# Kernel optimization log

Measured on AMD Instinct MI355X. Metric: run time of the kernel, lower is better.

The kernel has to match this reference:

```python
import jax, jax.numpy as jnp
import numpy as np

CODEBOOK_SIZE = 8192
CODEBOOK_DIM = 16
IN_DIM = 512


def setup_inputs() -> dict:
    key = jax.random.key(0)
    k1, k2, k3 = jax.random.split(key, 3)
    input_values = jax.random.normal(k1, (8, 4096, IN_DIM), dtype=jnp.float32)
    # xavier_uniform for Linear(IN_DIM -> CODEBOOK_DIM), weight shape (out, in) in torch
    limit = float(np.sqrt(6.0 / (IN_DIM + CODEBOOK_DIM)))
    proj_weight = jax.random.uniform(k2, (CODEBOOK_DIM, IN_DIM), dtype=jnp.float32, minval=-limit, maxval=limit)
    code_book = jax.random.normal(k3, (CODEBOOK_SIZE, CODEBOOK_DIM), dtype=jnp.float32)
    return {"input_values": input_values, "proj_weight": proj_weight, "code_book": code_book}


def reference(input_values, proj_weight, code_book):
    # targets: (B, L, d) = input @ W^T  (bias-free random projection)
    targets = jnp.einsum("bld,cd->blc", input_values, proj_weight)  # (B, L, 16)
    # Squared L2 distance via expansion ||t - c||^2 = ||t||^2 - 2 t.c + ||c||^2.
    # argmin is identical to argmin of the norm; avoids the (B,L,K,d) broadcast tensor.
    t_sq = jnp.sum(targets * targets, axis=-1, keepdims=True)        # (B, L, 1)
    c_sq = jnp.sum(code_book * code_book, axis=-1)                   # (K,)
    cross = jnp.einsum("blc,kc->blk", targets, code_book)            # (B, L, K)
    dist_sq = t_sq - 2.0 * cross + c_sq                              # (B, L, K)
    labels = jnp.argmin(dist_sq, axis=-1)                            # (B, L) int
    return labels
```

## Files before the change

### kernel.cpp

```cpp
#include <hip/hip_runtime.h>
#include <stdint.h>

#define IN_DIM 512
#define CB 8192
#define CD 16
#define NROWS 32768
#define DELTAQ 8e-3f
#define FMAXV 3.402823466e38f
#define FBB 4

typedef short bf16x8 __attribute__((ext_vector_type(8)));
typedef float f32x4 __attribute__((ext_vector_type(4)));

__device__ inline unsigned short f2bf(float x) {
    unsigned u = __float_as_uint(x);
    unsigned r = u + 0x7FFFu + ((u >> 16) & 1u);
    return (unsigned short)(r >> 16);
}
__device__ inline float bf2f(unsigned short h) { return __uint_as_float(((unsigned)h) << 16); }
__device__ inline unsigned umin32(unsigned a, unsigned b) { return a < b ? a : b; }
__device__ inline unsigned umax32(unsigned a, unsigned b) { return a > b ? a : b; }
__device__ inline unsigned long long shfl_xor_u64(unsigned long long x, int m) {
    double d = __shfl_xor(__longlong_as_double((long long)x), m, 64);
    return (unsigned long long)__double_as_longlong(d);
}
__device__ inline unsigned med3_u32(unsigned a, unsigned b, unsigned c) {
    unsigned d;
    asm("v_med3_u32 %0, %1, %2, %3" : "=v"(d) : "v"(a), "v"(b), "v"(c));
    return d;
}

__global__ __launch_bounds__(256) void prep_kernel(const float* __restrict__ cb,
                                                   float* __restrict__ csq,
                                                   f32x4* __restrict__ csq4,
                                                   bf16x8* __restrict__ Bp,
                                                   int* __restrict__ counter) {
    int id = blockIdx.x * 256 + threadIdx.x;
    if (id == 0) counter[0] = 0;
    if (id < CB) {
        const float4* p = (const float4*)(cb + (size_t)id * CD);
        float s = 0.f;
#pragma unroll
        for (int j = 0; j < 4; ++j) {
            float4 v = p[j];
            s += v.x * v.x + v.y * v.y + v.z * v.z + v.w * v.w;
        }
        csq[id] = s;
        float so = s + 256.0f;
        f32x4 v4 = {so, so, so, so};
        csq4[id] = v4;
    }
    int slot = id & 63;
    int nt = id >> 6;
    int q = slot >> 4;
    int n = nt * 16 + (slot & 15);
    int d0 = (q & 1) * 8;
    bool lo = (q < 2);
    const float* src = cb + (size_t)n * CD + d0;
    bf16x8 v;
#pragma unroll
    for (int j = 0; j < 8; ++j) {
        float x = src[j];
        unsigned short a = f2bf(x);
        unsigned short b = f2bf(x - bf2f(a));
        v[j] = (short)(lo ? a : b);
    }
    Bp[id] = v;
}

__global__ __launch_bounds__(512, 4) void fused_kernel(
        const float* __restrict__ in, const float* __restrict__ W,
        float* __restrict__ tpout, const f32x4* __restrict__ csq4,
        const bf16x8* __restrict__ Bp, int* __restrict__ out,
        int* __restrict__ queue, int* __restrict__ counter) {
    __shared__ float4 LIN[2048];
    __shared__ float4 WL[16 * 129];
    __shared__ float tbuf[64][17];
    __shared__ unsigned long long m_k[64][8];
    __shared__ unsigned m_s2[64][8];

    int tid = threadIdx.x;
    int lane = tid & 63;
    int wv = __builtin_amdgcn_readfirstlane(tid >> 6);
    int rowbase = blockIdx.x * 64;
    const float4* inp4 = (const float4*)in;
    const float4* W4 = (const float4*)W;

#pragma unroll
    for (int u = 0; u < 4; ++u) {
        int f = tid + u * 512;
        int d = f >> 7, k = f & 127;
        WL[d * 129 + k] = W4[(size_t)d * 128 + k];
    }

    float fold0 = 0.f, fold1 = 0.f;
    for (int c = 0; c < 4; ++c) {
        __syncthreads();
#pragma unroll
        for (int u = 0; u < 4; ++u) {
            int f = tid + u * 512;
            int o = f & 31, r = f >> 5;
            LIN[o * 64 + (r ^ (o & 7))] = inp4[(size_t)(rowbase + r) * 128 + c * 32 + o];
        }
        __syncthreads();
        float acc0 = 0.f, acc1 = 0.f;
#pragma unroll 4
        for (int j = 0; j < 32; ++j) {
            float4 v = LIN[j * 64 + (lane ^ (j & 7))];
            float4 w0 = WL[(2 * wv) * 129 + c * 32 + j];
            float4 w1 = WL[(2 * wv + 1) * 129 + c * 32 + j];
            acc0 += v.x * w0.x + v.y * w0.y + v.z * w0.z + v.w * w0.w;
            acc1 += v.x * w1.x + v.y * w1.y + v.z * w1.z + v.w * w1.w;
        }
        fold0 += acc0;
        fold1 += acc1;
    }
    float t0 = -2.f * fold0;
    float t1 = -2.f * fold1;
    tbuf[lane][2 * wv] = t0;
    tbuf[lane][2 * wv + 1] = t1;
    {
        float* tp = tpout + (size_t)(rowbase + lane) * CD + 2 * wv;
        tp[0] = t0;
        tp[1] = t1;
    }
    __syncthreads();

    int e = wv;
    int q = lane >> 4;
    int col = lane & 15;
    int d0 = (q & 1) * 8;
    bool lo = (q < 2);

    bf16x8 A1[4], A2[4];
#pragma unroll
    for (int g = 0; g < 4; ++g) {
        int arow = 16 * g + col;
#pragma unroll
        for (int j = 0; j < 8; ++j) {
            float x = tbuf[arow][d0 + j];
            unsigned short h1 = f2bf(x);
            unsigned short h2 = f2bf(x - bf2f(h1));
            A1[g][j] = (short)h1;
            A2[g][j] = (short)(lo ? h2 : 0);
        }
    }

    unsigned s1[4][4], s2[4][4];
#pragma unroll
    for (int g = 0; g < 4; ++g)
#pragma unroll
        for (int r = 0; r < 4; ++r) { s1[g][r] = 0xFFFFFFFFu; s2[g][r] = 0xFFFFFFFFu; }

    int nt0 = e * 64;
    const bf16x8* pb = Bp + (size_t)nt0 * 64 + lane;
    const f32x4* csqp = csq4 + nt0 * 16 + col;

    for (int tc = 0; tc < 16; ++tc) {
        bf16x8 bv[4];
        f32x4 iv[4];
#pragma unroll
        for (int u = 0; u < 4; ++u) {
            bv[u] = pb[u * 64];
            iv[u] = csqp[u * 16];
        }
#pragma unroll
        for (int u = 0; u < 4; ++u) {
            unsigned tt = (unsigned)(tc * 4 + u);
#pragma unroll
            for (int g = 0; g < 4; ++g) {
                f32x4 acc = __builtin_amdgcn_mfma_f32_16x16x32_bf16(A1[g], bv[u], iv[u], 0, 0, 0);
                acc = __builtin_amdgcn_mfma_f32_16x16x32_bf16(A2[g], bv[u], acc, 0, 0, 0);
#pragma unroll
                for (int r = 0; r < 4; ++r) {
                    unsigned k = (__float_as_uint(acc[r]) & 0xFFFFFFC0u) | tt;
                    s2[g][r] = med3_u32(s1[g][r], s2[g][r], k);
                    s1[g][r] = umin32(s1[g][r], k);
                }
            }
        }
        pb += 256;
        csqp += 64;
    }

#pragma unroll
    for (int g = 0; g < 4; ++g)
#pragma unroll
        for (int r = 0; r < 4; ++r) {
            unsigned long long FK = ((unsigned long long)(s1[g][r] & 0xFFFFFFC0u) << 13)
                                  | ((unsigned long long)e << 10)
                                  | ((unsigned long long)(s1[g][r] & 63u) << 4)
                                  | (unsigned long long)col;
            unsigned s2q = s2[g][r] & 0xFFFFFFC0u;
#pragma unroll
            for (int m = 1; m < 16; m <<= 1) {
                unsigned long long oFK = shfl_xor_u64(FK, m);
                unsigned os2 = (unsigned)__shfl_xor((int)s2q, m, 64);
                unsigned qa = (unsigned)(FK >> 13);
                unsigned qb = (unsigned)(oFK >> 13);
                s2q = umin32(umin32(s2q, os2), umax32(qa, qb));
                FK = oFK < FK ? oFK : FK;
            }
            if (col == 0) {
                int rl = 16 * g + 4 * q + r;
                m_k[rl][e] = FK;
                m_s2[rl][e] = s2q;
            }
        }
    __syncthreads();

    if (tid < 64) {
        unsigned long long mFK = m_k[tid][0];
        unsigned g1 = (unsigned)(m_k[tid][0] >> 13);
        unsigned g2 = m_s2[tid][0];
#pragma unroll
        for (int ee = 1; ee < 8; ++ee) {
            unsigned long long F = m_k[tid][ee];
            unsigned u = (unsigned)(F >> 13);
            if (u < g1) { g2 = g1; g1 = u; } else { g2 = umin32(g2, u); }
            g2 = umin32(g2, m_s2[tid][ee]);
            mFK = F < mFK ? F : mFK;
        }
        int ccol = (int)(mFK & 15ull);
        int ctile = (int)((mFK >> 4) & 63ull);
        int ce = (int)((mFK >> 10) & 7ull);
        int row = rowbase + tid;
        out[row] = ((ce * 64 + ctile) << 4) | ccol;
        if (__uint_as_float(g2) - __uint_as_float(g1) < DELTAQ) {
            int pos = atomicAdd(counter, 1);
            queue[pos] = row;
        }
    }
}

__global__ __launch_bounds__(256, 2) void fallback_kernel(const float* __restrict__ tpout,
                                                          const float* __restrict__ cb,
                                                          const float* __restrict__ csq,
                                                          const int* __restrict__ queue,
                                                          const int* __restrict__ counter,
                                                          int* __restrict__ out) {
    __shared__ float tps[FBB][16];
    __shared__ int rowsS[FBB];
    __shared__ unsigned long long red[4][FBB];
    int nq = counter[0];
    int tid = threadIdx.x;
    int lane = tid & 63;
    int w = tid >> 6;

    for (int qb = blockIdx.x * FBB; qb < nq; qb += 2048 * FBB) {
        if (tid < FBB) {
            int qi = qb + tid;
            rowsS[tid] = queue[qi < nq ? qi : nq - 1];
        }
        __syncthreads();
        if (tid < FBB * 16) {
            int r = tid >> 4, d = tid & 15;
            tps[r][d] = tpout[(size_t)rowsS[r] * CD + d];
        }
        __syncthreads();

        float tp[FBB][16];
#pragma unroll
        for (int r = 0; r < FBB; ++r)
#pragma unroll
            for (int d = 0; d < 16; ++d) tp[r][d] = tps[r][d];

        float best[FBB];
        int bidx[FBB];
#pragma unroll
        for (int r = 0; r < FBB; ++r) { best[r] = FMAXV; bidx[r] = 0; }

        for (int i = 0; i < 32; ++i) {
            int k = tid + 256 * i;
            const float* cp = cb + (size_t)k * CD;
            float cpr[16];
#pragma unroll
            for (int d = 0; d < 16; ++d) cpr[d] = cp[d];
            float cq = csq[k];
#pragma unroll
            for (int r = 0; r < FBB; ++r) {
                float s = cq;
#pragma unroll
                for (int d = 0; d < 16; ++d) s += tp[r][d] * cpr[d];
                if (s < best[r]) { best[r] = s; bidx[r] = k; }
            }
        }

#pragma unroll
        for (int r = 0; r < FBB; ++r) {
            unsigned u = __float_as_uint(best[r]);
            u = (u & 0x80000000u) ? ~u : (u | 0x80000000u);
            unsigned long long key = ((unsigned long long)u << 32) | (unsigned)bidx[r];
#pragma unroll
            for (int m = 1; m < 64; m <<= 1) {
                unsigned long long o = shfl_xor_u64(key, m);
                key = o < key ? o : key;
            }
            if (lane == 0) red[w][r] = key;
        }
        __syncthreads();
        if (tid < FBB) {
            unsigned long long mm = red[0][tid];
#pragma unroll
            for (int i2 = 1; i2 < 4; ++i2) { unsigned long long x = red[i2][tid]; mm = x < mm ? x : mm; }
            if (qb + tid < nq) out[rowsS[tid]] = (int)(mm & 0xFFFFFFFFull);
        }
        __syncthreads();
    }
}

extern "C" void kernel_launch(void* const* d_in, const int* in_sizes, int n_in,
                              void* d_out, int out_size, void* d_ws, size_t ws_size,
                              hipStream_t stream) {
    const float* input = (const float*)d_in[0];
    const float* W     = (const float*)d_in[1];
    const float* cb    = (const float*)d_in[2];
    int* out = (int*)d_out;

    float*  tpout   = (float*)d_ws;
    float*  csq     = tpout + (size_t)NROWS * CD;
    f32x4*  csq4    = (f32x4*)(csq + CB);
    bf16x8* Bp      = (bf16x8*)((float*)csq4 + 4 * CB);
    int*    counter = (int*)(Bp + 32768);
    int*    queue   = counter + 16;

    prep_kernel<<<32768 / 256, 256, 0, stream>>>(cb, csq, csq4, Bp, counter);
    fused_kernel<<<NROWS / 64, 512, 0, stream>>>(input, W, tpout, csq4, Bp, out, queue, counter);
    fallback_kernel<<<2048, 256, 0, stream>>>(tpout, cb, csq, queue, counter, out);
}
```

Before: 177.3 us.

## Fuse exact fallback rescoring into main kernel, drop global queue and third launch

Ambiguous rows, where the top-two approximate distances are within a margin, are now collected per block in shared memory with a ballot and popcount. The same block then rescores them exactly in fp32 against the full codebook. This replaces the global atomic queue, the tpout workspace writes and the separate fallback kernel launch. The cost is that blocks with many ambiguous rows serialize this work at the tail of the fused kernel, possibly unevenly, and the extra shared memory and registers may reduce occupancy.

```diff
diff --git a/kernel.cpp b/kernel.cpp
--- a/kernel.cpp
+++ b/kernel.cpp
@@ -7,7 +7,6 @@
 #define NROWS 32768
 #define DELTAQ 8e-3f
 #define FMAXV 3.402823466e38f
-#define FBB 4
 
 typedef short bf16x8 __attribute__((ext_vector_type(8)));
 typedef float f32x4 __attribute__((ext_vector_type(4)));
@@ -33,10 +32,8 @@
 __global__ __launch_bounds__(256) void prep_kernel(const float* __restrict__ cb,
                                                    float* __restrict__ csq,
                                                    f32x4* __restrict__ csq4,
-                                                   bf16x8* __restrict__ Bp,
-                                                   int* __restrict__ counter) {
+                                                   bf16x8* __restrict__ Bp) {
     int id = blockIdx.x * 256 + threadIdx.x;
-    if (id == 0) counter[0] = 0;
     if (id < CB) {
         const float4* p = (const float4*)(cb + (size_t)id * CD);
         float s = 0.f;
@@ -70,14 +67,17 @@
 
 __global__ __launch_bounds__(512, 4) void fused_kernel(
         const float* __restrict__ in, const float* __restrict__ W,
-        float* __restrict__ tpout, const f32x4* __restrict__ csq4,
-        const bf16x8* __restrict__ Bp, int* __restrict__ out,
-        int* __restrict__ queue, int* __restrict__ counter) {
+        const float* __restrict__ cb, const float* __restrict__ csq,
+        const f32x4* __restrict__ csq4, const bf16x8* __restrict__ Bp,
+        int* __restrict__ out) {
     __shared__ float4 LIN[2048];
     __shared__ float4 WL[16 * 129];
     __shared__ float tbuf[64][17];
     __shared__ unsigned long long m_k[64][8];
     __shared__ unsigned m_s2[64][8];
+    __shared__ int qrows[64];
+    __shared__ int qn;
+    __shared__ unsigned long long redq[8][4];
 
     int tid = threadIdx.x;
     int lane = tid & 63;
@@ -115,15 +115,8 @@
         fold0 += acc0;
         fold1 += acc1;
     }
-    float t0 = -2.f * fold0;
-    float t1 = -2.f * fold1;
-    tbuf[lane][2 * wv] = t0;
-    tbuf[lane][2 * wv + 1] = t1;
-    {
-        float* tp = tpout + (size_t)(rowbase + lane) * CD + 2 * wv;
-        tp[0] = t0;
-        tp[1] = t1;
-    }
+    tbuf[lane][2 * wv] = -2.f * fold0;
+    tbuf[lane][2 * wv + 1] = -2.f * fold1;
     __syncthreads();
 
     int e = wv;
@@ -224,61 +217,42 @@
         int ccol = (int)(mFK & 15ull);
         int ctile = (int)((mFK >> 4) & 63ull);
         int ce = (int)((mFK >> 10) & 7ull);
-        int row = rowbase + tid;
-        out[row] = ((ce * 64 + ctile) << 4) | ccol;
-        if (__uint_as_float(g2) - __uint_as_float(g1) < DELTAQ) {
-            int pos = atomicAdd(counter, 1);
-            queue[pos] = row;
-        }
-    }
-}
-
-__global__ __launch_bounds__(256, 2) void fallback_kernel(const float* __restrict__ tpout,
-                                                          const float* __restrict__ cb,
-                                                          const float* __restrict__ csq,
-                                                          const int* __restrict__ queue,
-                                                          const int* __restrict__ counter,
-                                                          int* __restrict__ out) {
-    __shared__ float tps[FBB][16];
-    __shared__ int rowsS[FBB];
-    __shared__ unsigned long long red[4][FBB];
-    int nq = counter[0];
-    int tid = threadIdx.x;
-    int lane = tid & 63;
-    int w = tid >> 6;
-
-    for (int qb = blockIdx.x * FBB; qb < nq; qb += 2048 * FBB) {
-        if (tid < FBB) {
-            int qi = qb + tid;
-            rowsS[tid] = queue[qi < nq ? qi : nq - 1];
-        }
-        __syncthreads();
-        if (tid < FBB * 16) {
-            int r = tid >> 4, d = tid & 15;
-            tps[r][d] = tpout[(size_t)rowsS[r] * CD + d];
-        }
-        __syncthreads();
-
-        float tp[FBB][16];
-#pragma unroll
-        for (int r = 0; r < FBB; ++r)
-#pragma unroll
-            for (int d = 0; d < 16; ++d) tp[r][d] = tps[r][d];
-
-        float best[FBB];
-        int bidx[FBB];
-#pragma unroll
-        for (int r = 0; r < FBB; ++r) { best[r] = FMAXV; bidx[r] = 0; }
-
-        for (int i = 0; i < 32; ++i) {
-            int k = tid + 256 * i;
+        out[rowbase + tid] = ((ce * 64 + ctile) << 4) | ccol;
+        bool amb = (__uint_as_float(g2) - __uint_as_float(g1) < DELTAQ);
+        unsigned long long mask = __ballot(amb);
+        if (amb) {
+            int pos = __popcll(mask & ((1ull << tid) - 1ull));
+            qrows[pos] = tid;
+        }
+        if (tid == 0) qn = (int)__popcll(mask);
+    }
+    __syncthreads();
+
+    int nqb = qn;
+    for (int q0 = 0; q0 < nqb; q0 += 4) {
+        int rr[4];
+#pragma unroll
+        for (int r = 0; r < 4; ++r) rr[r] = qrows[(q0 + r < nqb) ? q0 + r : nqb - 1];
+        float tp[4][16];
+#pragma unroll
+        for (int r = 0; r < 4; ++r)
+#pragma unroll
+            for (int d = 0; d < 16; ++d) tp[r][d] = tbuf[rr[r]][d];
+
+        float best[4];
+        int bidx[4];
+#pragma unroll
+        for (int r = 0; r < 4; ++r) { best[r] = FMAXV; bidx[r] = 0; }
+
+        for (int i = 0; i < 16; ++i) {
+            int k = tid + 512 * i;
             const float* cp = cb + (size_t)k * CD;
             float cpr[16];
 #pragma unroll
             for (int d = 0; d < 16; ++d) cpr[d] = cp[d];
             float cq = csq[k];
 #pragma unroll
-            for (int r = 0; r < FBB; ++r) {
+            for (int r = 0; r < 4; ++r) {
                 float s = cq;
 #pragma unroll
                 for (int d = 0; d < 16; ++d) s += tp[r][d] * cpr[d];
@@ -287,7 +261,7 @@
         }
 
 #pragma unroll
-        for (int r = 0; r < FBB; ++r) {
+        for (int r = 0; r < 4; ++r) {
             unsigned u = __float_as_uint(best[r]);
             u = (u & 0x80000000u) ? ~u : (u | 0x80000000u);
             unsigned long long key = ((unsigned long long)u << 32) | (unsigned)bidx[r];
@@ -296,14 +270,14 @@
                 unsigned long long o = shfl_xor_u64(key, m);
                 key = o < key ? o : key;
             }
-            if (lane == 0) red[w][r] = key;
+            if (lane == 0) redq[wv][r] = key;
         }
         __syncthreads();
-        if (tid < FBB) {
-            unsigned long long mm = red[0][tid];
-#pragma unroll
-            for (int i2 = 1; i2 < 4; ++i2) { unsigned long long x = red[i2][tid]; mm = x < mm ? x : mm; }
-            if (qb + tid < nq) out[rowsS[tid]] = (int)(mm & 0xFFFFFFFFull);
+        if (tid < 4 && q0 + tid < nqb) {
+            unsigned long long mm = redq[0][tid];
+#pragma unroll
+            for (int i2 = 1; i2 < 8; ++i2) { unsigned long long x = redq[i2][tid]; mm = x < mm ? x : mm; }
+            out[rowbase + qrows[q0 + tid]] = (int)(mm & 0xFFFFFFFFull);
         }
         __syncthreads();
     }
@@ -317,14 +291,10 @@
     const float* cb    = (const float*)d_in[2];
     int* out = (int*)d_out;
 
-    float*  tpout   = (float*)d_ws;
-    float*  csq     = tpout + (size_t)NROWS * CD;
-    f32x4*  csq4    = (f32x4*)(csq + CB);
-    bf16x8* Bp      = (bf16x8*)((float*)csq4 + 4 * CB);
-    int*    counter = (int*)(Bp + 32768);
-    int*    queue   = counter + 16;
-
-    prep_kernel<<<32768 / 256, 256, 0, stream>>>(cb, csq, csq4, Bp, counter);
-    fused_kernel<<<NROWS / 64, 512, 0, stream>>>(input, W, tpout, csq4, Bp, out, queue, counter);
-    fallback_kernel<<<2048, 256, 0, stream>>>(tpout, cb, csq, queue, counter, out);
-}
+    float*  csq  = (float*)d_ws;
+    f32x4*  csq4 = (f32x4*)(csq + CB);
+    bf16x8* Bp   = (bf16x8*)((float*)csq4 + 4 * CB);
+
+    prep_kernel<<<32768 / 256, 256, 0, stream>>>(cb, csq, csq4, Bp);
+    fused_kernel<<<NROWS / 64, 512, 0, stream>>>(input, W, cb, csq, csq4, Bp, out);
+}
```

Result: faster. 165.0 us (-6.9%).
